# Kernel tuning notes

Hardware: AMD Instinct MI355X
Metric: run time of the kernel (lower is better)

The kernel has to match this reference:

```python
import jax, jax.numpy as jnp
import numpy as np

HOPS = 2
BN_EPS = 1e-5


def _glorot(key, shape):
    fan_in = shape[-2]
    bound = 1.0 / np.sqrt(fan_in)
    return jax.random.uniform(key, shape, jnp.float32, -bound, bound)


def setup_inputs() -> dict:
    key = jax.random.key(0)
    ks = jax.random.split(key, 12)
    n, e = 50000, 800000
    in_c, hid, out_c = 128, 96, 64
    x = jax.random.normal(ks[0], (n, in_c), jnp.float32)
    edge_index = jax.random.randint(ks[1], (2, e), 0, n, jnp.int32)
    # MixHopLayer 0: hops+1 linears in_c -> hid (stacked)
    conv0_W = _glorot(ks[2], (HOPS + 1, in_c, hid))
    conv0_b = jnp.zeros((HOPS + 1, hid), jnp.float32)
    # MixHopLayer 1: hops+1 linears hid*(hops+1) -> out_c
    conv1_W = _glorot(ks[3], (HOPS + 1, hid * (HOPS + 1), out_c))
    conv1_b = jnp.zeros((HOPS + 1, out_c), jnp.float32)
    # BatchNorm1d(hid*(hops+1)) eval-mode params/buffers
    w = hid * (HOPS + 1)
    bn_gamma = jnp.ones((w,), jnp.float32)
    bn_beta = jnp.zeros((w,), jnp.float32)
    bn_mean = 0.1 * jax.random.normal(ks[4], (w,), jnp.float32)
    bn_var = jnp.ones((w,), jnp.float32) + 0.1 * jax.random.uniform(ks[5], (w,))
    # final projection out_c*(hops+1) -> out_c
    fp_W = _glorot(ks[6], (out_c * (HOPS + 1), out_c))
    fp_b = jnp.zeros((out_c,), jnp.float32)
    return dict(x=x, edge_index=edge_index, conv0_W=conv0_W, conv0_b=conv0_b,
                conv1_W=conv1_W, conv1_b=conv1_b, bn_gamma=bn_gamma, bn_beta=bn_beta,
                bn_mean=bn_mean, bn_var=bn_var, fp_W=fp_W, fp_b=fp_b)


def _gcn_norm(edge_index, n):
    # PyG gcn_norm with add_self_loops=True, improved=False, symmetric norm.
    row, col = edge_index[0], edge_index[1]
    loop = jnp.arange(n, dtype=edge_index.dtype)
    row = jnp.concatenate([row, loop])
    col = jnp.concatenate([col, loop])
    deg = jax.ops.segment_sum(jnp.ones_like(col, jnp.float32), col, num_segments=n)
    dinv = jnp.where(deg > 0, jax.lax.rsqrt(deg), 0.0)
    w = dinv[row] * dinv[col]
    return row, col, w


def _spmm_adj_t(row, col, w, x, n):
    # adj_t = SparseTensor(row=col, col=row, value=w): out[col] += w * x[row]
    return jax.ops.segment_sum(w[:, None] * x[row], col, num_segments=n)


def _mixhop_layer(x, W, b, row, col, w, n):
    xs = [x @ W[0] + b[0]]
    for j in range(1, HOPS + 1):
        xj = x @ W[j] + b[j]
        for _ in range(j):
            xj = _spmm_adj_t(row, col, w, xj, n)
        xs.append(xj)
    return jnp.concatenate(xs, axis=1)


def reference(x, edge_index, conv0_W, conv0_b, conv1_W, conv1_b,
              bn_gamma, bn_beta, bn_mean, bn_var, fp_W, fp_b):
    n = x.shape[0]
    row, col, w = _gcn_norm(edge_index, n)
    h = _mixhop_layer(x, conv0_W, conv0_b, row, col, w, n)
    # BatchNorm1d (eval) + ReLU; dropout is identity in eval
    h = bn_gamma * (h - bn_mean) * jax.lax.rsqrt(bn_var + BN_EPS) + bn_beta
    h = jax.nn.relu(h)
    h = _mixhop_layer(h, conv1_W, conv1_b, row, col, w, n)
    return h @ fp_W + fp_b
```

## Files before the change

### kernel.cpp

```cpp
#include <hip/hip_runtime.h>

#define IN_C 128
#define HID 96
#define OUT_C 64
#define W0C 288
#define W1C 192
#define CAP 5120
#define EPB 4096

typedef __bf16 bf16x8v __attribute__((ext_vector_type(8)));
typedef float  f32x4v  __attribute__((ext_vector_type(4)));

__global__ void k_combo_prep(const float* __restrict__ x, __bf16* __restrict__ xb, int n8,
                             const float* __restrict__ W0, const float* __restrict__ W1,
                             const float* __restrict__ Wf,
                             const float* __restrict__ gamma, const float* __restrict__ beta,
                             const float* __restrict__ mean, const float* __restrict__ var,
                             __bf16* __restrict__ w0t, __bf16* __restrict__ w1t,
                             __bf16* __restrict__ wft,
                             float* __restrict__ scale, float* __restrict__ shift,
                             int* __restrict__ zp, int nz,
                             int CB, int PB) {
    int b = blockIdx.x;
    if (b < CB) {
        int i = b * 256 + threadIdx.x;
        if (i >= n8) return;
        bf16x8v o;
#pragma unroll
        for (int q = 0; q < 8; q++) o[q] = (__bf16)x[i * 8 + q];
        *(bf16x8v*)(xb + (size_t)i * 8) = o;
    } else if (b < CB + PB) {
        const int T0 = 3 * IN_C * HID;
        const int T1 = 3 * W0C * OUT_C;
        const int T2 = W1C * OUT_C;
        int i = (b - CB) * 256 + threadIdx.x;
        if (i < T0) {
            int kn = IN_C * HID;
            int j = i / kn, r = i % kn;
            int k = r / HID, nn = r % HID;
            w0t[(size_t)j * kn + (size_t)nn * IN_C + k] = (__bf16)W0[i];
        } else if (i < T0 + T1) {
            int ii = i - T0;
            int kn = W0C * OUT_C;
            int j = ii / kn, r = ii % kn;
            int k = r / OUT_C, nn = r % OUT_C;
            w1t[(size_t)j * kn + (size_t)nn * W0C + k] = (__bf16)W1[ii];
        } else if (i < T0 + T1 + T2) {
            int ii = i - T0 - T1;
            int k = ii / OUT_C, nn = ii % OUT_C;
            wft[(size_t)nn * W1C + k] = (__bf16)Wf[ii];
        } else if (i < T0 + T1 + T2 + W0C) {
            int ii = i - T0 - T1 - T2;
            float s = gamma[ii] * rsqrtf(var[ii] + 1e-5f);
            scale[ii] = s;
            shift[ii] = beta[ii] - mean[ii] * s;
        }
    } else {
        int i = (b - CB - PB) * 256 + threadIdx.x;
        if (i < nz) zp[i] = 0;
    }
}

__global__ __launch_bounds__(256) void k_mega0(
        const int* __restrict__ row, const int* __restrict__ col,
        int* __restrict__ counts, int* __restrict__ bcur ,
        int2* __restrict__ binned, int e, int SB,
        const __bf16* __restrict__ xb, const __bf16* __restrict__ w0t ,
        const float* __restrict__ bias , __bf16* __restrict__ h,
        const float* __restrict__ scale, const float* __restrict__ shift, int M) {
    const int RS = 104;
    __shared__ __bf16 tile[128 * RS];
    int tid = threadIdx.x;
    if ((int)blockIdx.x < SB) {
        int* hist  = (int*)tile;
        int* basep = hist + 256;
        int e0 = blockIdx.x * EPB;
        int cnt = min(EPB, e - e0);
        hist[tid] = 0;
        __syncthreads();
        int rr[16], cc[16], rk[16];
#pragma unroll
        for (int k = 0; k < 16; k++) {
            int idx = tid + k * 256;
            if (idx < cnt) {
                rr[k] = row[e0 + idx];
                cc[k] = col[e0 + idx];
                atomicAdd(&counts[cc[k]], 1);
                rk[k] = atomicAdd(&hist[cc[k] >> 8], 1);
            }
        }
        __syncthreads();
        {
            int hv = hist[tid];
            if (hv > 0) basep[tid] = atomicAdd(&bcur[tid * 16], hv);
        }
        __syncthreads();
#pragma unroll
        for (int k = 0; k < 16; k++) {
            int idx = tid + k * 256;
            if (idx < cnt) {
                int b = cc[k] >> 8;
                int pos = basep[b] + rk[k];
                if (pos < CAP)
                    binned[(size_t)b * CAP + pos] = make_int2(rr[k], cc[k]);
            }
        }
        return;
    }
    int wave = tid >> 6, lane = tid & 63;
    int ln = lane & 15, quad = lane >> 4;
    int rowBase = (blockIdx.x - SB) * 128;
    int waveRow = wave * 16;
    f32x4v acc[2][6];
#pragma unroll
    for (int u = 0; u < 2; u++)
#pragma unroll
        for (int t = 0; t < 6; t++) acc[u][t] = (f32x4v){0.f, 0.f, 0.f, 0.f};
    const __bf16* arow0 = xb + (size_t)(rowBase + waveRow + ln) * IN_C + quad * 8;
    const __bf16* arow1 = arow0 + (size_t)64 * IN_C;
#pragma unroll
    for (int k = 0; k < 4; k++) {
        bf16x8v a0 = *(const bf16x8v*)(arow0 + k * 32);
        bf16x8v a1 = *(const bf16x8v*)(arow1 + k * 32);
#pragma unroll
        for (int c = 0; c < 6; c++) {
            bf16x8v b = *(const bf16x8v*)(w0t + (size_t)(c * 16 + ln) * IN_C + k * 32 + quad * 8);
            acc[0][c] = __builtin_amdgcn_mfma_f32_16x16x32_bf16(a0, b, acc[0][c], 0, 0, 0);
            acc[1][c] = __builtin_amdgcn_mfma_f32_16x16x32_bf16(a1, b, acc[1][c], 0, 0, 0);
        }
    }
#pragma unroll
    for (int u = 0; u < 2; u++)
#pragma unroll
        for (int r = 0; r < 4; r++) {
            int lr = u * 64 + waveRow + quad * 4 + r;
#pragma unroll
            for (int c = 0; c < 6; c++) {
                int col2 = c * 16 + ln;
                float v = acc[u][c][r] + bias[col2];
                v = fmaxf(v * scale[col2] + shift[col2], 0.f);
                tile[lr * RS + col2] = (__bf16)v;
            }
        }
    __syncthreads();
#pragma unroll
    for (int s = 0; s < 6; s++) {
        int idx = tid + s * 256;
        int r = idx / 12, c8 = idx % 12;
        int grow = rowBase + r;
        if (grow < M)
            *(bf16x8v*)(h + (size_t)grow * W0C + c8 * 8) =
                *(const bf16x8v*)(tile + r * RS + c8 * 8);
    }
}

__global__ void k_dinv_scan(const int* __restrict__ counts, const int* __restrict__ bcur,
                            float* __restrict__ dinv, int* __restrict__ bscan,
                            int n, int nb) {
    if (blockIdx.x == 0) {
        __shared__ int s[256];
        int v = ((int)threadIdx.x < nb) ? bcur[threadIdx.x * 16] : 0;
        s[threadIdx.x] = v;
        __syncthreads();
        for (int off = 1; off < 256; off <<= 1) {
            int t = ((int)threadIdx.x >= off) ? s[threadIdx.x - off] : 0;
            __syncthreads();
            s[threadIdx.x] += t;
            __syncthreads();
        }
        if ((int)threadIdx.x < nb) bscan[threadIdx.x] = s[threadIdx.x] - v;
    } else {
        int i = (blockIdx.x - 1) * 256 + threadIdx.x;
        if (i < n) dinv[i] = rsqrtf((float)(counts[i] + 1));
    }
}

__global__ __launch_bounds__(256) void k_bucket_sort(
        const int2* __restrict__ binned, const int* __restrict__ counts,
        const int* __restrict__ bcur, const int* __restrict__ bscan,
        const float* __restrict__ dinv,
        int2* __restrict__ csr, int* __restrict__ row_ptr,
        float* __restrict__ arow, int n) {
    __shared__ int   s_src[CAP];
    __shared__ int   s_col[CAP];
    __shared__ int   s_ofs[256];
    __shared__ int   lcur[256];
    __shared__ float s_a[256];
    int tid = threadIdx.x;
    int node0 = blockIdx.x << 8;
    int base = bscan[blockIdx.x];
    int cnt  = min(bcur[blockIdx.x * 16], CAP);
    const int2* bin = binned + (size_t)blockIdx.x * CAP;

    int node = node0 + tid;
    int cdeg = (node < n) ? counts[node] : 0;
    s_ofs[tid] = cdeg;
    __syncthreads();
    for (int o = 1; o < 256; o <<= 1) {
        int u = (tid >= o) ? s_ofs[tid - o] : 0;
        __syncthreads();
        s_ofs[tid] += u;
        __syncthreads();
    }
    int nodeOfs = s_ofs[tid] - cdeg;
    if (node < n) {
        row_ptr[node] = base + nodeOfs;
        if (node == n - 1) row_ptr[n] = base + nodeOfs + cdeg;
    }
    lcur[tid] = 0;
    __syncthreads();
    for (int t = tid; t < cnt; t += 256)
        atomicAdd(&lcur[bin[t].x >> 8], 1);
    __syncthreads();
    {
        int v = lcur[tid];
        s_ofs[tid] = v;
        __syncthreads();
        for (int o = 1; o < 256; o <<= 1) {
            int u = (tid >= o) ? s_ofs[tid - o] : 0;
            __syncthreads();
            s_ofs[tid] += u;
            __syncthreads();
        }
        lcur[tid] = s_ofs[tid] - v;
    }
    __syncthreads();
    for (int t = tid; t < cnt; t += 256) {
        int2 rc = bin[t];
        int pos = atomicAdd(&lcur[rc.x >> 8], 1);
        s_src[pos] = rc.x;
        s_col[pos] = rc.y;
    }
    __syncthreads();
    s_ofs[tid] = nodeOfs;
    lcur[tid] = 0;
    s_a[tid] = 0.f;
    __syncthreads();
    for (int t = tid; t < cnt; t += 256) {
        int r = s_src[t], c = s_col[t];
        int local = c - node0;
        int pos = s_ofs[local] + atomicAdd(&lcur[local], 1);
        float wv = dinv[r] * dinv[c];
        csr[base + pos] = make_int2(r, __float_as_int(wv));
        atomicAdd(&s_a[local], wv);
    }
    __syncthreads();
    if (node < n) {
        float d = dinv[node];
        arow[node] = s_a[tid] + d * d;
    }
}


__global__ __launch_bounds__(256) void k_mf_l0b(
        const __bf16* __restrict__ s1, const __bf16* __restrict__ w0t,
        const float* __restrict__ bias , const float* __restrict__ arow,
        __bf16* __restrict__ h, __bf16* __restrict__ tp,
        const float* __restrict__ scale, const float* __restrict__ shift, int M) {
    const int RS = 104;
    __shared__ __bf16 tile[64 * RS];
    int tid = threadIdx.x;
    int wave = tid >> 6, lane = tid & 63;
    int ln = lane & 15, quad = lane >> 4;
    int rowBase = blockIdx.x * 64;
    int waveRow = wave * 16;
    const __bf16* w1p = w0t + (size_t)1 * HID * IN_C;
    const __bf16* w2p = w0t + (size_t)2 * HID * IN_C;
    f32x4v acc[2][6];
#pragma unroll
    for (int j = 0; j < 2; j++)
#pragma unroll
        for (int t = 0; t < 6; t++) acc[j][t] = (f32x4v){0.f, 0.f, 0.f, 0.f};
    const __bf16* arow0 = s1 + (size_t)(rowBase + waveRow + ln) * IN_C + quad * 8;
#pragma unroll
    for (int k = 0; k < 4; k++) {
        bf16x8v a0 = *(const bf16x8v*)(arow0 + k * 32);
#pragma unroll
        for (int c = 0; c < 6; c++) {
            bf16x8v b1 = *(const bf16x8v*)(w1p + (size_t)(c * 16 + ln) * IN_C + k * 32 + quad * 8);
            bf16x8v b2 = *(const bf16x8v*)(w2p + (size_t)(c * 16 + ln) * IN_C + k * 32 + quad * 8);
            acc[0][c] = __builtin_amdgcn_mfma_f32_16x16x32_bf16(a0, b1, acc[0][c], 0, 0, 0);
            acc[1][c] = __builtin_amdgcn_mfma_f32_16x16x32_bf16(a0, b2, acc[1][c], 0, 0, 0);
        }
    }
    float avs[4];
#pragma unroll
    for (int r = 0; r < 4; r++)
        avs[r] = arow[rowBase + waveRow + quad * 4 + r];
#pragma unroll
    for (int jj = 0; jj < 2; jj++) {
        const float* bj = bias + (jj + 1) * HID;
#pragma unroll
        for (int r = 0; r < 4; r++) {
            int lr = waveRow + quad * 4 + r;
            float av = avs[r];
#pragma unroll
            for (int c = 0; c < 6; c++) {
                int col = c * 16 + ln;
                float v = acc[jj][c][r] + av * bj[col];
                if (jj == 0) v = fmaxf(v * scale[HID + col] + shift[HID + col], 0.f);
                tile[lr * RS + col] = (__bf16)v;
            }
        }
        __syncthreads();
#pragma unroll
        for (int s = 0; s < 3; s++) {
            int idx = tid + s * 256;
            int r = idx / 12, c8 = idx % 12;
            int grow = rowBase + r;
            if (grow < M) {
                __bf16* dst = (jj == 0) ? (h + (size_t)grow * W0C + HID)
                                        : (tp + (size_t)grow * HID);
                *(bf16x8v*)(dst + c8 * 8) = *(const bf16x8v*)(tile + r * RS + c8 * 8);
            }
        }
        __syncthreads();
    }
}

__global__ __launch_bounds__(256) void k_mf_l1m(
        const __bf16* __restrict__ hb, const __bf16* __restrict__ w1t ,
        const float* __restrict__ bias ,
        __bf16* __restrict__ g, __bf16* __restrict__ u12, int M) {
    const int RS = 72;
    __shared__ __bf16 tile[64 * RS];
    int tid = threadIdx.x;
    int wave = tid >> 6, lane = tid & 63;
    int ln = lane & 15, quad = lane >> 4;
    int rowBase = blockIdx.x * 64;
    int waveRow = wave * 16;
    f32x4v acc[3][4];
#pragma unroll
    for (int j = 0; j < 3; j++)
#pragma unroll
        for (int t = 0; t < 4; t++) acc[j][t] = (f32x4v){0.f, 0.f, 0.f, 0.f};
    const __bf16* arow0 = hb + (size_t)(rowBase + waveRow + ln) * W0C + quad * 8;
#pragma unroll
    for (int k = 0; k < 9; k++) {
        bf16x8v a0 = *(const bf16x8v*)(arow0 + k * 32);
#pragma unroll
        for (int c = 0; c < 4; c++) {
#pragma unroll
            for (int j = 0; j < 3; j++) {
                bf16x8v b = *(const bf16x8v*)(w1t + (size_t)j * OUT_C * W0C +
                                              (size_t)(c * 16 + ln) * W0C + k * 32 + quad * 8);
                acc[j][c] = __builtin_amdgcn_mfma_f32_16x16x32_bf16(a0, b, acc[j][c], 0, 0, 0);
            }
        }
    }
#pragma unroll
    for (int j = 0; j < 3; j++) {
        const float* bj = bias + j * OUT_C;
#pragma unroll
        for (int r = 0; r < 4; r++) {
            int lr = waveRow + quad * 4 + r;
#pragma unroll
            for (int c = 0; c < 4; c++) {
                int col = c * 16 + ln;
                tile[lr * RS + col] = (__bf16)(acc[j][c][r] + bj[col]);
            }
        }
        __syncthreads();
        __bf16* dst = (j == 0) ? g : u12;
        int ld = (j == 0) ? W1C : 128;
        int c0 = (j == 2) ? OUT_C : 0;
#pragma unroll
        for (int s = 0; s < 2; s++) {
            int idx = tid + s * 256;
            int r = idx / 8, c8 = idx % 8;
            int grow = rowBase + r;
            if (grow < M)
                *(bf16x8v*)(dst + (size_t)grow * ld + c0 + c8 * 8) =
                    *(const bf16x8v*)(tile + r * RS + c8 * 8);
        }
        __syncthreads();
    }
}

__global__ __launch_bounds__(256) void k_mf_fin(
        const __bf16* __restrict__ gb, const __bf16* __restrict__ wft ,
        const float* __restrict__ bias, float* __restrict__ out, int M) {
    const int RS = 68;
    __shared__ float tile[128 * RS];
    int tid = threadIdx.x;
    int wave = tid >> 6, lane = tid & 63;
    int ln = lane & 15, quad = lane >> 4;
    int rowBase = blockIdx.x * 128;
    int waveRow = wave * 16;
    f32x4v acc[2][4];
#pragma unroll
    for (int u = 0; u < 2; u++)
#pragma unroll
        for (int t = 0; t < 4; t++) acc[u][t] = (f32x4v){0.f, 0.f, 0.f, 0.f};
    const __bf16* arow0 = gb + (size_t)(rowBase + waveRow + ln) * W1C + quad * 8;
    const __bf16* arow1 = arow0 + (size_t)64 * W1C;
#pragma unroll
    for (int k = 0; k < 6; k++) {
        bf16x8v a0 = *(const bf16x8v*)(arow0 + k * 32);
        bf16x8v a1 = *(const bf16x8v*)(arow1 + k * 32);
#pragma unroll
        for (int c = 0; c < 4; c++) {
            bf16x8v b = *(const bf16x8v*)(wft + (size_t)(c * 16 + ln) * W1C + k * 32 + quad * 8);
            acc[0][c] = __builtin_amdgcn_mfma_f32_16x16x32_bf16(a0, b, acc[0][c], 0, 0, 0);
            acc[1][c] = __builtin_amdgcn_mfma_f32_16x16x32_bf16(a1, b, acc[1][c], 0, 0, 0);
        }
    }
#pragma unroll
    for (int u = 0; u < 2; u++)
#pragma unroll
        for (int r = 0; r < 4; r++) {
            int lr = u * 64 + waveRow + quad * 4 + r;
#pragma unroll
            for (int c = 0; c < 4; c++) {
                int col = c * 16 + ln;
                tile[lr * RS + col] = acc[u][c][r] + bias[col];
            }
        }
    __syncthreads();
#pragma unroll
    for (int s = 0; s < 8; s++) {
        int idx = tid + s * 256;
        int r = idx / 16, c4 = idx % 16;
        int grow = rowBase + r;
        if (grow < M)
            *(float4*)(out + (size_t)grow * OUT_C + c4 * 4) =
                *(const float4*)(tile + r * RS + c4 * 4);
    }
}

template <int C8, int NPB, bool BNRELU>
__global__ void k_spmm(const __bf16* __restrict__ xin, int ldx,
                       __bf16* __restrict__ xout, int ldo,
                       const int* __restrict__ row_ptr, const int* __restrict__ counts,
                       const int2* __restrict__ csr,
                       const float* __restrict__ dinv, int n,
                       const float* __restrict__ scale, const float* __restrict__ shift,
                       int chan0) {
    int c8 = threadIdx.x % C8;
    int nl = threadIdx.x / C8;
    int node = blockIdx.x * NPB + nl;
    if (node >= n) return;
    float di = dinv[node];
    float lw = di * di;
    float acc[8];
    {
        bf16x8v v = *(const bf16x8v*)(xin + (size_t)node * ldx + c8 * 8);
#pragma unroll
        for (int q = 0; q < 8; q++) acc[q] = lw * (float)v[q];
    }
    int start = row_ptr[node];
    int cnt = counts[node];
    int k = 0;
    for (; k + 4 <= cnt; k += 4) {
        int2 p0 = csr[start + k + 0], p1 = csr[start + k + 1];
        int2 p2 = csr[start + k + 2], p3 = csr[start + k + 3];
        float w0 = __int_as_float(p0.y), w1 = __int_as_float(p1.y);
        float w2 = __int_as_float(p2.y), w3 = __int_as_float(p3.y);
        bf16x8v v0 = *(const bf16x8v*)(xin + (size_t)p0.x * ldx + c8 * 8);
        bf16x8v v1 = *(const bf16x8v*)(xin + (size_t)p1.x * ldx + c8 * 8);
        bf16x8v v2 = *(const bf16x8v*)(xin + (size_t)p2.x * ldx + c8 * 8);
        bf16x8v v3 = *(const bf16x8v*)(xin + (size_t)p3.x * ldx + c8 * 8);
#pragma unroll
        for (int q = 0; q < 8; q++)
            acc[q] += w0 * (float)v0[q] + w1 * (float)v1[q] +
                      w2 * (float)v2[q] + w3 * (float)v3[q];
    }
    for (; k < cnt; k++) {
        int2 p = csr[start + k];
        float w = __int_as_float(p.y);
        bf16x8v xv = *(const bf16x8v*)(xin + (size_t)p.x * ldx + c8 * 8);
#pragma unroll
        for (int q = 0; q < 8; q++) acc[q] += w * (float)xv[q];
    }
    bf16x8v o;
#pragma unroll
    for (int q = 0; q < 8; q++) {
        float v = acc[q];
        if (BNRELU) {
            int ch = chan0 + c8 * 8 + q;
            v = fmaxf(v * scale[ch] + shift[ch], 0.f);
        }
        o[q] = (__bf16)v;
    }
    *(bf16x8v*)(xout + (size_t)node * ldo + c8 * 8) = o;
}

template <int C8, int SPLIT, int NPB, bool BNA, bool BNB>
__global__ void k_spmm2(const __bf16* __restrict__ xin, int ldx,
                        __bf16* __restrict__ dstA, int ldA, int chanA,
                        __bf16* __restrict__ dstB, int ldB, int chanB,
                        const int* __restrict__ row_ptr, const int* __restrict__ counts,
                        const int2* __restrict__ csr,
                        const float* __restrict__ dinv, int n,
                        const float* __restrict__ scale, const float* __restrict__ shift) {
    int c8 = threadIdx.x % C8;
    int nl = threadIdx.x / C8;
    int node = blockIdx.x * NPB + nl;
    if (node >= n) return;
    float di = dinv[node];
    float lw = di * di;
    float acc[8];
    {
        bf16x8v v = *(const bf16x8v*)(xin + (size_t)node * ldx + c8 * 8);
#pragma unroll
        for (int q = 0; q < 8; q++) acc[q] = lw * (float)v[q];
    }
    int start = row_ptr[node];
    int cnt = counts[node];
    int k = 0;
    for (; k + 4 <= cnt; k += 4) {
        int2 p0 = csr[start + k + 0], p1 = csr[start + k + 1];
        int2 p2 = csr[start + k + 2], p3 = csr[start + k + 3];
        float w0 = __int_as_float(p0.y), w1 = __int_as_float(p1.y);
        float w2 = __int_as_float(p2.y), w3 = __int_as_float(p3.y);
        bf16x8v v0 = *(const bf16x8v*)(xin + (size_t)p0.x * ldx + c8 * 8);
        bf16x8v v1 = *(const bf16x8v*)(xin + (size_t)p1.x * ldx + c8 * 8);
        bf16x8v v2 = *(const bf16x8v*)(xin + (size_t)p2.x * ldx + c8 * 8);
        bf16x8v v3 = *(const bf16x8v*)(xin + (size_t)p3.x * ldx + c8 * 8);
#pragma unroll
        for (int q = 0; q < 8; q++)
            acc[q] += w0 * (float)v0[q] + w1 * (float)v1[q] +
                      w2 * (float)v2[q] + w3 * (float)v3[q];
    }
    for (; k < cnt; k++) {
        int2 p = csr[start + k];
        float w = __int_as_float(p.y);
        bf16x8v xv = *(const bf16x8v*)(xin + (size_t)p.x * ldx + c8 * 8);
#pragma unroll
        for (int q = 0; q < 8; q++) acc[q] += w * (float)xv[q];
    }
    bool isA = c8 < SPLIT;
    __bf16* dst = isA ? dstA : dstB;
    int ld   = isA ? ldA : ldB;
    int lc8  = isA ? c8 : c8 - SPLIT;
    int chan = isA ? chanA : chanB;
    bool bn  = isA ? BNA : BNB;
    bf16x8v o;
#pragma unroll
    for (int q = 0; q < 8; q++) {
        float v = acc[q];
        if (bn) {
            int ch = chan + lc8 * 8 + q;
            v = fmaxf(v * scale[ch] + shift[ch], 0.f);
        }
        o[q] = (__bf16)v;
    }
    *(bf16x8v*)(dst + (size_t)node * ld + lc8 * 8) = o;
}


extern "C" void kernel_launch(void* const* d_in, const int* in_sizes, int n_in,
                              void* d_out, int out_size, void* d_ws, size_t ws_size,
                              hipStream_t stream) {
    const int n = in_sizes[0] / IN_C;
    const int e = in_sizes[1] / 2;

    const float* x    = (const float*)d_in[0];
    const int*   ei   = (const int*)d_in[1];
    const float* W0   = (const float*)d_in[2];
    const float* b0   = (const float*)d_in[3];
    const float* W1   = (const float*)d_in[4];
    const float* b1   = (const float*)d_in[5];
    const float* bn_g = (const float*)d_in[6];
    const float* bn_b = (const float*)d_in[7];
    const float* bn_m = (const float*)d_in[8];
    const float* bn_v = (const float*)d_in[9];
    const float* Wf   = (const float*)d_in[10];
    const float* bf   = (const float*)d_in[11];
    float* out = (float*)d_out;

    const int* e_row = ei;
    const int* e_col = ei + e;

    char* ws = (char*)d_ws;
    size_t off = 0;
    auto alloc = [&](size_t bytes) -> void* {
        void* p = ws + off;
        off += (bytes + 255) & ~(size_t)255;
        return p;
    };
    const int NP = n + 128;
    int nb = (n + 255) / 256;

    int*    counts  = (int*)alloc((size_t)(n + 256 * 16) * 4);
    int*    bcur    = counts + n;
    int*    row_ptr = (int*)alloc((size_t)(n + 1) * 4);
    int*    bscan   = (int*)alloc(256 * 4);
    float*  dinv    = (float*)alloc((size_t)n * 4);
    float*  arow    = (float*)alloc((size_t)NP * 4);
    int2*   binned  = (int2*)alloc((size_t)nb * CAP * 8);
    int2*   csr     = (int2*)alloc((size_t)e * 8);
    float*  bnscale = (float*)alloc(W0C * 4);
    float*  bnshift = (float*)alloc(W0C * 4);
    __bf16* xb  = (__bf16*)alloc((size_t)NP * IN_C * 2);
    __bf16* w0t = (__bf16*)alloc((size_t)3 * HID * IN_C * 2);
    __bf16* w1t = (__bf16*)alloc((size_t)3 * OUT_C * W0C * 2);
    __bf16* wft = (__bf16*)alloc((size_t)OUT_C * W1C * 2);
    __bf16* s1  = (__bf16*)alloc((size_t)NP * 128 * 2);
    __bf16* tp  = (__bf16*)alloc((size_t)NP * HID * 2);
    __bf16* h   = (__bf16*)alloc((size_t)NP * W0C * 2);
    __bf16* g   = (__bf16*)alloc((size_t)NP * W1C * 2);
    __bf16* u12 = s1;
    __bf16* up  = tp;

    int n8 = n * IN_C / 8;
    int nz = n + 256 * 16;
    int ptotal = 3 * IN_C * HID + 3 * W0C * OUT_C + W1C * OUT_C + W0C;
    int CB = (n8 + 255) / 256;
    int PB = (ptotal + 255) / 256;
    int ZB = (nz + 255) / 256;
    k_combo_prep<<<dim3(CB + PB + ZB), dim3(256), 0, stream>>>(
        x, xb, n8, W0, W1, Wf, bn_g, bn_b, bn_m, bn_v,
        w0t, w1t, wft, bnscale, bnshift, counts, nz, CB, PB);

    int SB = (e + EPB - 1) / EPB;
    int GG = (n + 127) / 128;
    k_mega0<<<dim3(SB + GG), dim3(256), 0, stream>>>(
        e_row, e_col, counts, bcur, binned, e, SB,
        xb, w0t, b0, h, bnscale, bnshift, n);

    k_dinv_scan<<<dim3(1 + nb), dim3(256), 0, stream>>>(counts, bcur, dinv, bscan, n, nb);

    k_bucket_sort<<<dim3(nb), dim3(256), 0, stream>>>(binned, counts, bcur, bscan, dinv,
                                                      csr, row_ptr, arow, n);

    dim3 g64((n + 63) / 64);

    k_spmm<16, 16, false><<<dim3((n + 15) / 16), dim3(256), 0, stream>>>(
        xb, IN_C, s1, 128, row_ptr, counts, csr, dinv, n, nullptr, nullptr, 0);
    k_mf_l0b<<<g64, dim3(256), 0, stream>>>(s1, w0t, b0, arow, h, tp, bnscale, bnshift, n);
    k_spmm<12, 16, true><<<dim3((n + 15) / 16), dim3(192), 0, stream>>>(
        tp, HID, h + 2 * HID, W0C, row_ptr, counts, csr, dinv, n,
        bnscale, bnshift, 2 * HID);

    k_mf_l1m<<<g64, dim3(256), 0, stream>>>(h, w1t, b1, g, u12, n);

    k_spmm2<16, 8, 16, false, false><<<dim3((n + 15) / 16), dim3(256), 0, stream>>>(
        u12, 128, g + OUT_C, W1C, 0, up, OUT_C, 0,
        row_ptr, counts, csr, dinv, n, nullptr, nullptr);
    k_spmm<8, 32, false><<<dim3((n + 31) / 32), dim3(256), 0, stream>>>(
        up, OUT_C, g + 2 * OUT_C, W1C, row_ptr, counts, csr, dinv, n,
        nullptr, nullptr, 0);

    k_mf_fin<<<dim3((n + 127) / 128), dim3(256), 0, stream>>>(g, wft, bf, out, n);
}
```

Baseline: 328.3 us.

## Compute node degrees from binned edges in shared memory instead of global atomics

Removes the per-edge global atomicAdd on the counts array from the binning pass. Degrees are now recomputed in a new per-bucket kernel that histograms the binned column indices with shared-memory atomics and writes counts and dinv. Edges per binning block shrink from 4096 to 1024, giving more blocks with fewer registers each. The cost is one extra read of the binned edge array, plus more global atomics on the bucket cursors because there are more binning blocks.

```diff
diff --git a/kernel.cpp b/kernel.cpp
--- a/kernel.cpp
+++ b/kernel.cpp
@@ -6,7 +6,7 @@
 #define W0C 288
 #define W1C 192
 #define CAP 5120
-#define EPB 4096
+#define EPB 1024
 
 typedef __bf16 bf16x8v __attribute__((ext_vector_type(8)));
 typedef float  f32x4v  __attribute__((ext_vector_type(4)));
@@ -63,7 +63,7 @@
 
 __global__ __launch_bounds__(256) void k_mega0(
         const int* __restrict__ row, const int* __restrict__ col,
-        int* __restrict__ counts, int* __restrict__ bcur ,
+        int* __restrict__ bcur ,
         int2* __restrict__ binned, int e, int SB,
         const __bf16* __restrict__ xb, const __bf16* __restrict__ w0t ,
         const float* __restrict__ bias , __bf16* __restrict__ h,
@@ -78,14 +78,13 @@
         int cnt = min(EPB, e - e0);
         hist[tid] = 0;
         __syncthreads();
-        int rr[16], cc[16], rk[16];
-#pragma unroll
-        for (int k = 0; k < 16; k++) {
+        int rr[4], cc[4], rk[4];
+#pragma unroll
+        for (int k = 0; k < 4; k++) {
             int idx = tid + k * 256;
             if (idx < cnt) {
                 rr[k] = row[e0 + idx];
                 cc[k] = col[e0 + idx];
-                atomicAdd(&counts[cc[k]], 1);
                 rk[k] = atomicAdd(&hist[cc[k] >> 8], 1);
             }
         }
@@ -96,7 +95,7 @@
         }
         __syncthreads();
 #pragma unroll
-        for (int k = 0; k < 16; k++) {
+        for (int k = 0; k < 4; k++) {
             int idx = tid + k * 256;
             if (idx < cnt) {
                 int b = cc[k] >> 8;
@@ -154,24 +153,36 @@
     }
 }
 
-__global__ void k_dinv_scan(const int* __restrict__ counts, const int* __restrict__ bcur,
-                            float* __restrict__ dinv, int* __restrict__ bscan,
-                            int n, int nb) {
-    if (blockIdx.x == 0) {
-        __shared__ int s[256];
-        int v = ((int)threadIdx.x < nb) ? bcur[threadIdx.x * 16] : 0;
-        s[threadIdx.x] = v;
+__global__ void k_deg_scan(const int2* __restrict__ binned, const int* __restrict__ bcur,
+                           int* __restrict__ counts, float* __restrict__ dinv,
+                           int* __restrict__ bscan, int n, int nb) {
+    __shared__ int s[256];
+    int tid = threadIdx.x;
+    if ((int)blockIdx.x == nb) {
+        int v = (tid < nb) ? bcur[tid * 16] : 0;
+        s[tid] = v;
         __syncthreads();
         for (int off = 1; off < 256; off <<= 1) {
-            int t = ((int)threadIdx.x >= off) ? s[threadIdx.x - off] : 0;
+            int t = (tid >= off) ? s[tid - off] : 0;
             __syncthreads();
-            s[threadIdx.x] += t;
+            s[tid] += t;
             __syncthreads();
         }
-        if ((int)threadIdx.x < nb) bscan[threadIdx.x] = s[threadIdx.x] - v;
-    } else {
-        int i = (blockIdx.x - 1) * 256 + threadIdx.x;
-        if (i < n) dinv[i] = rsqrtf((float)(counts[i] + 1));
+        if (tid < nb) bscan[tid] = s[tid] - v;
+        return;
+    }
+    s[tid] = 0;
+    __syncthreads();
+    int cnt = min(bcur[blockIdx.x * 16], CAP);
+    const int2* bin = binned + (size_t)blockIdx.x * CAP;
+    for (int t = tid; t < cnt; t += 256)
+        atomicAdd(&s[bin[t].y & 255], 1);
+    __syncthreads();
+    int node = (blockIdx.x << 8) + tid;
+    if (node < n) {
+        int d = s[tid];
+        counts[node] = d;
+        dinv[node] = rsqrtf((float)(d + 1));
     }
 }
 
@@ -604,22 +615,23 @@
     __bf16* up  = tp;
 
     int n8 = n * IN_C / 8;
-    int nz = n + 256 * 16;
+    int nz = 256 * 16;
     int ptotal = 3 * IN_C * HID + 3 * W0C * OUT_C + W1C * OUT_C + W0C;
     int CB = (n8 + 255) / 256;
     int PB = (ptotal + 255) / 256;
     int ZB = (nz + 255) / 256;
     k_combo_prep<<<dim3(CB + PB + ZB), dim3(256), 0, stream>>>(
         x, xb, n8, W0, W1, Wf, bn_g, bn_b, bn_m, bn_v,
-        w0t, w1t, wft, bnscale, bnshift, counts, nz, CB, PB);
+        w0t, w1t, wft, bnscale, bnshift, bcur, nz, CB, PB);
 
     int SB = (e + EPB - 1) / EPB;
     int GG = (n + 127) / 128;
     k_mega0<<<dim3(SB + GG), dim3(256), 0, stream>>>(
-        e_row, e_col, counts, bcur, binned, e, SB,
+        e_row, e_col, bcur, binned, e, SB,
         xb, w0t, b0, h, bnscale, bnshift, n);
 
-    k_dinv_scan<<<dim3(1 + nb), dim3(256), 0, stream>>>(counts, bcur, dinv, bscan, n, nb);
+    k_deg_scan<<<dim3(nb + 1), dim3(256), 0, stream>>>(binned, bcur, counts, dinv,
+                                                       bscan, n, nb);
 
     k_bucket_sort<<<dim3(nb), dim3(256), 0, stream>>>(binned, counts, bcur, bscan, dinv,
                                                       csr, row_ptr, arow, n);
```

New measurement: 321.4 us. 1.02x faster.
